# Kernel tuning notes

Hardware: AMD Instinct MI355X
Metric: run time of the kernel (lower is better)

The kernel has to match this reference:

```python
import jax, jax.numpy as jnp
import numpy as np

B, S, D = 4, 2048, 1024
H, HD = 16, 64
SCALE = 1.0 / np.sqrt(HD)


def setup_inputs() -> dict:
    key = jax.random.key(0)
    k1, k2, k3 = jax.random.split(key, 3)
    std = 0.02
    return {
        "hidden_states": jax.random.normal(k1, (B, S, D), jnp.float32),
        "attention_mask": jnp.ones((B, S), dtype=bool),
        "w_attn": jax.random.normal(k2, (D, 3 * D), jnp.float32) * std,
        "b_attn": jnp.zeros((3 * D,), jnp.float32),
        "w_proj": jax.random.normal(k3, (D, D), jnp.float32) * std,
        "b_proj": jnp.zeros((D,), jnp.float32),
    }


def reference(hidden_states, attention_mask, w_attn, b_attn, w_proj, b_proj):
    b, s, _ = hidden_states.shape
    qkv = hidden_states @ w_attn + b_attn                     # [B,S,3D]
    q, k, v = jnp.split(qkv, 3, axis=-1)
    # [B,H,S,HD]
    q = q.reshape(b, s, H, HD).transpose(0, 2, 1, 3)
    k = k.reshape(b, s, H, HD).transpose(0, 2, 1, 3)
    v = v.reshape(b, s, H, HD).transpose(0, 2, 1, 3)
    scores = jnp.einsum('bhqd,bhkd->bhqk', q, k) * SCALE      # [B,H,S,S]
    causal = jnp.tril(jnp.ones((s, s), dtype=bool))
    scores = jnp.where(causal, scores, -jnp.inf)
    scores = jnp.where(attention_mask[:, None, None, :], scores, -jnp.inf)
    probs = jax.nn.softmax(scores, axis=-1)
    out = jnp.einsum('bhqk,bhkd->bhqd', probs, v)             # [B,H,S,HD]
    out = out.transpose(0, 2, 1, 3).reshape(b, s, H * HD)
    return out @ w_proj + b_proj
```

## Files before the change

### kernel.cpp

```cpp
#include <hip/hip_runtime.h>
#include <hip/hip_bf16.h>
#include <stdint.h>

#define B_ 4
#define S_ 2048
#define D_ 1024
#define H_ 16
#define HD_ 64
#define TD_ 3072
#define SCALE_ 0.125f
#define SC2_ 0.18033688011112042f
#define KVB 64
#define QB 128

typedef __attribute__((ext_vector_type(4))) float f32x4;
typedef __attribute__((ext_vector_type(16))) float f32x16;
typedef __attribute__((ext_vector_type(8))) short s16x8;
typedef __attribute__((ext_vector_type(8))) unsigned short u16x8;
typedef __attribute__((ext_vector_type(4))) unsigned int u32x4;

typedef const __attribute__((address_space(1))) unsigned int* gas1p;
typedef __attribute__((address_space(3))) unsigned int* as3p;

__device__ inline void gload_lds16(const void* g, void* l) {
    __builtin_amdgcn_global_load_lds((gas1p)g, (as3p)l, 16, 0, 0);
}

__device__ inline unsigned short f2bf(float f) {
    unsigned u = __builtin_bit_cast(unsigned, f);
    u += 0x7FFFu + ((u >> 16) & 1u);
    return (unsigned short)(u >> 16);
}
__device__ inline float bf2f(unsigned short b) {
    unsigned u = ((unsigned)b) << 16;
    return __builtin_bit_cast(float, u);
}
__device__ inline unsigned cvtpk_bf16(float lo, float hi) {
    unsigned r;
    asm("v_cvt_pk_bf16_f32 %0, %1, %2" : "=v"(r) : "v"(lo), "v"(hi));
    return r;
}
__device__ inline float ex2(float x) { return __builtin_amdgcn_exp2f(x); }

__global__ void sniff_kernel(const unsigned* __restrict__ x, int* __restrict__ flag) {
    int lane = threadIdx.x;
    int cnt = 0;
#pragma unroll
    for (int i = 0; i < 8; i++) {
        unsigned e = (x[lane * 8 + i] >> 7) & 0xFFu;
        cnt += (e > 100u && e < 140u) ? 1 : 0;
    }
    cnt += __shfl_xor(cnt, 1);
    cnt += __shfl_xor(cnt, 2);
    cnt += __shfl_xor(cnt, 4);
    cnt += __shfl_xor(cnt, 8);
    cnt += __shfl_xor(cnt, 16);
    cnt += __shfl_xor(cnt, 32);
    if (lane == 0) *flag = (cnt > 300) ? 1 : 0;
}

__global__ void cvt_bf16_kernel(const void* __restrict__ in, unsigned short* __restrict__ out,
                                long n8, const int* __restrict__ flag) {
    bool isbf = (*flag) != 0;
    long i = (long)blockIdx.x * blockDim.x + threadIdx.x;
    long stride = (long)gridDim.x * blockDim.x;
    for (; i < n8; i += stride) {
        if (isbf) {
            ((u32x4*)out)[i] = ((const u32x4*)in)[i];
        } else {
            const float* f = (const float*)in + i * 8;
            u16x8 r;
#pragma unroll
            for (int j = 0; j < 8; j++) r[j] = f2bf(f[j]);
            ((u16x8*)out)[i] = r;
        }
    }
}

__global__ void tcvt2_kernel(const void* __restrict__ in0, unsigned short* __restrict__ out0,
                             const void* __restrict__ in1, unsigned short* __restrict__ out1,
                             const int* __restrict__ flag) {
    int z = blockIdx.z;
    int bx = blockIdx.x, by = blockIdx.y;
    if (z == 1 && bx >= 32) return;
    const void* in = z ? in1 : in0;
    unsigned short* out = z ? out1 : out0;
    int R = 1024;
    int C = z ? 1024 : 3072;
    bool isbf = (*flag) != 0;
    __shared__ unsigned short tile[32][33];
    int x = threadIdx.x, y0 = threadIdx.y;
    int c = bx * 32 + x;
    for (int yy = y0; yy < 32; yy += 8) {
        long r = by * 32 + yy;
        unsigned short v;
        if (isbf) v = ((const unsigned short*)in)[r * C + c];
        else      v = f2bf(((const float*)in)[r * C + c]);
        tile[yy][x] = v;
    }
    __syncthreads();
    for (int yy = y0; yy < 32; yy += 8) {
        out[(long)(bx * 32 + yy) * R + by * 32 + x] = tile[x][yy];
    }
}

__global__ void cvt_bias_kernel(const void* __restrict__ in0, float* __restrict__ out0,
                                const void* __restrict__ in1, float* __restrict__ out1,
                                const int* __restrict__ flag) {
    bool isbf = (*flag) != 0;
    int i = blockIdx.x * blockDim.x + threadIdx.x;
    if (i < 3072) {
        out0[i] = isbf ? bf2f(((const unsigned short*)in0)[i]) : ((const float*)in0)[i];
    } else if (i < 4096) {
        int j = i - 3072;
        out1[j] = isbf ? bf2f(((const unsigned short*)in1)[j]) : ((const float*)in1)[j];
    }
}

__global__ __launch_bounds__(512)
void vtrans_kernel(const unsigned short* __restrict__ QKV, unsigned short* __restrict__ Vt) {
    __shared__ unsigned short tile[64][72];
    int t = threadIdx.x;
    int st = blockIdx.x;
    int bh = blockIdx.y;
    int b = bh >> 4, h = bh & 15;
    const unsigned short* src = QKV + (long)b * S_ * TD_ + 2 * D_ + h * HD_;
    int sr = t >> 3, d0 = (t & 7) * 8;
    u16x8 v = *(const u16x8*)(src + (long)(st * 64 + sr) * TD_ + d0);
    *(u16x8*)&tile[sr][d0] = v;
    __syncthreads();
    int dr = t >> 3, s0 = (t & 7) * 8;
    u16x8 o;
#pragma unroll
    for (int j = 0; j < 8; j++) o[j] = tile[s0 + j][dr];
    *(u16x8*)(Vt + ((long)bh * 64 + dr) * S_ + st * 64 + s0) = o;
}

__global__ __launch_bounds__(256)
void gemm_bt_kernel(const unsigned short* __restrict__ A,
                    const unsigned short* __restrict__ Bt,
                    const float* __restrict__ bias,
                    void* __restrict__ Cout,
                    int M, int N, int K, const int* __restrict__ flag) {
    __shared__ unsigned short As[128 * 32];
    __shared__ unsigned short Bs[128 * 32];
    int t = threadIdx.x;
    int lane = t & 63;
    int w = t >> 6, wr = w >> 1, wc = w & 1;
    int g = lane >> 4, x = lane & 15;

    int nbx = gridDim.x, nby = gridDim.y;
    int nwg = nbx * nby;
    int orig = blockIdx.x + nbx * blockIdx.y;
    int per = nwg >> 3;
    int idx = (orig & 7) * per + (orig >> 3);
    int bx = idx / nby;
    int by = idx - bx * nby;

    long rm = (long)bx * 128;
    long rn = (long)by * 128;
    const char* Ab = (const char*)(A + rm * K);
    const char* Bb = (const char*)(Bt + rn * K);
    int r0 = t >> 2;
    int c0 = (t & 3) * 16;
    long Kb = (long)K * 2;

    f32x4 acc[4][4] = {};

    for (int k0 = 0; k0 < K; k0 += 32) {
        __syncthreads();
        long kb = (long)k0 * 2;
        gload_lds16(Ab + (long)r0 * Kb + kb + c0,        (char*)As + t * 16);
        gload_lds16(Ab + (long)(r0 + 64) * Kb + kb + c0, (char*)As + t * 16 + 4096);
        gload_lds16(Bb + (long)r0 * Kb + kb + c0,        (char*)Bs + t * 16);
        gload_lds16(Bb + (long)(r0 + 64) * Kb + kb + c0, (char*)Bs + t * 16 + 4096);
        __syncthreads();

        s16x8 af[4], bfr[4];
#pragma unroll
        for (int m = 0; m < 4; m++) af[m]  = *(const s16x8*)&As[(wr * 64 + m * 16 + x) * 32 + g * 8];
#pragma unroll
        for (int n = 0; n < 4; n++) bfr[n] = *(const s16x8*)&Bs[(wc * 64 + n * 16 + x) * 32 + g * 8];
#pragma unroll
        for (int m = 0; m < 4; m++)
#pragma unroll
            for (int n = 0; n < 4; n++)
                acc[m][n] = __builtin_amdgcn_mfma_f32_16x16x32_bf16(af[m], bfr[n], acc[m][n], 0, 0, 0);
    }

    bool f32out = flag ? ((*flag) == 0) : false;
    float bv[4];
#pragma unroll
    for (int n = 0; n < 4; n++) bv[n] = bias[rn + wc * 64 + n * 16 + x];

#pragma unroll
    for (int m = 0; m < 4; m++) {
#pragma unroll
        for (int r = 0; r < 4; r++) {
            long row = rm + wr * 64 + m * 16 + g * 4 + r;
            if (f32out) {
                float* cp = (float*)Cout + row * N;
#pragma unroll
                for (int n = 0; n < 4; n++) cp[rn + wc * 64 + n * 16 + x] = acc[m][n][r] + bv[n];
            } else {
                unsigned short* cp = (unsigned short*)Cout + row * N;
#pragma unroll
                for (int n = 0; n < 4; n++) cp[rn + wc * 64 + n * 16 + x] = f2bf(acc[m][n][r] + bv[n]);
            }
        }
    }
}

__global__ __launch_bounds__(256)
void attn_kernel(const unsigned short* __restrict__ QKV,
                 const unsigned short* __restrict__ Vt_g,
                 unsigned short* __restrict__ O) {
    __shared__ unsigned short Ks[2][64 * 64];
    __shared__ unsigned short Vs[2][64 * 64];

    int t = threadIdx.x, lane = t & 63, w = t >> 6;
    int hi = lane >> 5, q32 = lane & 31;
    int b = blockIdx.z, h = blockIdx.y;
    int pair = blockIdx.x;

    const unsigned short* base = QKV + (long)b * S_ * TD_;
    const unsigned short* Kb = base + D_ + h * HD_;
    const unsigned short* Vb = Vt_g + (long)(b * H_ + h) * HD_ * S_;

    int srow = t >> 3;
    int scol = (((t & 7) ^ (srow & 7)) << 3);

#define STAGE(bi, kt_)                                                            \
    {                                                                             \
        int ks_ = (kt_) * KVB;                                                    \
        gload_lds16(Kb + (long)(ks_ + srow) * TD_ + scol,      (char*)Ks[bi] + t * 16);          \
        gload_lds16(Kb + (long)(ks_ + 32 + srow) * TD_ + scol, (char*)Ks[bi] + 4096 + t * 16);   \
        gload_lds16(Vb + (long)srow * S_ + ks_ + scol,         (char*)Vs[bi] + t * 16);          \
        gload_lds16(Vb + (long)(32 + srow) * S_ + ks_ + scol,  (char*)Vs[bi] + 4096 + t * 16);   \
    }

    for (int ph = 0; ph < 2; ph++) {
        int qt = ph ? (15 - pair) : pair;
        int q0 = qt * QB;
        int q0w = q0 + w * 32;
        int nt = 2 * qt + 2;
        int wlimit = q0w + 31;
        int qg = q0w + q32;

        s16x8 qf[4];
        {
            const unsigned short* qr = base + (long)(q0w + q32) * TD_ + h * HD_;
#pragma unroll
            for (int ds = 0; ds < 4; ds++) {
                u16x8 qraw = *(const u16x8*)(qr + ds * 16 + hi * 8);
                u16x8 qs;
#pragma unroll
                for (int j = 0; j < 8; j++) qs[j] = f2bf(bf2f(qraw[j]) * SC2_);
                qf[ds] = __builtin_bit_cast(s16x8, qs);
            }
        }

        f32x16 acc0 = {}, acc1 = {};
        float sv[8] = {};

        STAGE(0, 0);
        __syncthreads();

        for (int kt = 0; kt < nt; kt++) {
            int bi = kt & 1;
            int ks = kt * KVB;
            if (kt + 1 < nt) STAGE(bi ^ 1, kt + 1);

            if (ks <= wlimit) {
                const char* KsB = (const char*)Ks[bi];
                const char* VsB = (const char*)Vs[bi];

                f32x16 sf0 = {}, sf1 = {};
                __builtin_amdgcn_s_setprio(1);
#pragma unroll
                for (int ds = 0; ds < 4; ds++) {
                    int krow0 = q32;
                    int krow1 = 32 + q32;
                    s16x8 kf0 = *(const s16x8*)(KsB + krow0 * 128 + (((ds * 2 + hi) ^ (krow0 & 7)) << 4));
                    s16x8 kf1 = *(const s16x8*)(KsB + krow1 * 128 + (((ds * 2 + hi) ^ (krow1 & 7)) << 4));
                    sf0 = __builtin_amdgcn_mfma_f32_32x32x16_bf16(kf0, qf[ds], sf0, 0, 0, 0);
                    sf1 = __builtin_amdgcn_mfma_f32_32x32x16_bf16(kf1, qf[ds], sf1, 0, 0, 0);
                }
                __builtin_amdgcn_s_setprio(0);

                if (ks + 63 > q0w) {
#pragma unroll
                    for (int r = 0; r < 16; r++) {
                        int koff = (r & 3) + 8 * (r >> 2) + 4 * hi;
                        if (ks + koff > qg)      sf0[r] = -__builtin_inff();
                        if (ks + 32 + koff > qg) sf1[r] = -__builtin_inff();
                    }
                }

#pragma unroll
                for (int r = 0; r < 16; r++) {
                    sf0[r] = ex2(sf0[r]);
                    sf1[r] = ex2(sf1[r]);
                }
#pragma unroll
                for (int r = 0; r < 8; r++)
                    sv[r] += (sf0[r] + sf0[r + 8]) + (sf1[r] + sf1[r + 8]);

                __builtin_amdgcn_s_setprio(1);
#pragma unroll
                for (int kst = 0; kst < 4; kst++) {
                    unsigned w00, w01, w10, w11;
                    if (kst == 0) { w00=cvtpk_bf16(sf0[0],sf0[1]);  w01=cvtpk_bf16(sf0[2],sf0[3]);
                                    w10=cvtpk_bf16(sf0[4],sf0[5]);  w11=cvtpk_bf16(sf0[6],sf0[7]); }
                    else if (kst == 1) { w00=cvtpk_bf16(sf0[8],sf0[9]);   w01=cvtpk_bf16(sf0[10],sf0[11]);
                                         w10=cvtpk_bf16(sf0[12],sf0[13]); w11=cvtpk_bf16(sf0[14],sf0[15]); }
                    else if (kst == 2) { w00=cvtpk_bf16(sf1[0],sf1[1]);  w01=cvtpk_bf16(sf1[2],sf1[3]);
                                         w10=cvtpk_bf16(sf1[4],sf1[5]);  w11=cvtpk_bf16(sf1[6],sf1[7]); }
                    else { w00=cvtpk_bf16(sf1[8],sf1[9]);   w01=cvtpk_bf16(sf1[10],sf1[11]);
                           w10=cvtpk_bf16(sf1[12],sf1[13]); w11=cvtpk_bf16(sf1[14],sf1[15]); }
                    auto sA = __builtin_amdgcn_permlane32_swap(w00, w10, false, false);
                    auto sB = __builtin_amdgcn_permlane32_swap(w01, w11, false, false);
                    union { unsigned u[4]; s16x8 v; } pa;
                    pa.u[0] = sA[0]; pa.u[1] = sB[0]; pa.u[2] = sA[1]; pa.u[3] = sB[1];

                    int d0 = q32;
                    int d1 = 32 + q32;
                    s16x8 vf0 = *(const s16x8*)(VsB + d0 * 128 + (((kst * 2 + hi) ^ (d0 & 7)) << 4));
                    s16x8 vf1 = *(const s16x8*)(VsB + d1 * 128 + (((kst * 2 + hi) ^ (d1 & 7)) << 4));
                    acc0 = __builtin_amdgcn_mfma_f32_32x32x16_bf16(pa.v, vf0, acc0, 0, 0, 0);
                    acc1 = __builtin_amdgcn_mfma_f32_32x32x16_bf16(pa.v, vf1, acc1, 0, 0, 0);
                }
                __builtin_amdgcn_s_setprio(0);
            }
            __syncthreads();
        }

        float dl = ((sv[0] + sv[1]) + (sv[2] + sv[3])) + ((sv[4] + sv[5]) + (sv[6] + sv[7]));
        float denom = dl + __shfl_xor(dl, 32);
        float inv = 1.0f / denom;

#pragma unroll
        for (int r = 0; r < 16; r++) {
            int crow = (r & 3) + 8 * (r >> 2) + 4 * hi;
            float ir = __shfl(inv, crow);
            long row = (long)b * S_ + q0w + crow;
            O[row * D_ + h * HD_ + q32]      = f2bf(acc0[r] * ir);
            O[row * D_ + h * HD_ + 32 + q32] = f2bf(acc1[r] * ir);
        }
    }
#undef STAGE
}

extern "C" void kernel_launch(void* const* d_in, const int* in_sizes, int n_in,
                              void* d_out, int out_size, void* d_ws, size_t ws_size,
                              hipStream_t stream) {
    char* ws = (char*)d_ws;
    int* flag            = (int*)ws;
    unsigned short* Xb   = (unsigned short*)(ws + 256);
    unsigned short* W1t  = Xb + 8192L * 1024;
    unsigned short* QKV  = W1t + 3072L * 1024;
    unsigned short* W2t  = QKV + 8192L * 3072;
    unsigned short* Ob   = W2t + 1024L * 1024;
    unsigned short* Vt_g = Ob + 8192L * 1024;
    float* b1            = (float*)(Vt_g + 64L * 64 * 2048);
    float* b2            = b1 + 3072;

    sniff_kernel<<<1, 64, 0, stream>>>((const unsigned*)d_in[0], flag);

    cvt_bf16_kernel<<<2048, 256, 0, stream>>>(d_in[0], Xb, 8192L * 1024 / 8, flag);
    tcvt2_kernel<<<dim3(96, 32, 2), dim3(32, 8), 0, stream>>>(d_in[2], W1t, d_in[4], W2t, flag);
    cvt_bias_kernel<<<16, 256, 0, stream>>>(d_in[3], b1, d_in[5], b2, flag);

    gemm_bt_kernel<<<dim3(64, 24), 256, 0, stream>>>(Xb, W1t, b1, QKV, 8192, 3072, 1024, nullptr);

    vtrans_kernel<<<dim3(32, 64), 512, 0, stream>>>(QKV, Vt_g);

    attn_kernel<<<dim3(8, 16, 4), 256, 0, stream>>>(QKV, Vt_g, Ob);

    gemm_bt_kernel<<<dim3(64, 8), 256, 0, stream>>>(Ob, W2t, b2, d_out, 8192, 1024, 1024, flag);
}
```

Measured before the change: 282.3 us.

## Fuse V transpose into QKV GEMM epilogue, swizzle LDS, skip bf16 copy

Removes the separate V-transpose kernel by having the QKV GEMM write V tiles straight into the transposed Vt buffer from its epilogue. It also adds an XOR swizzle to the GEMM's LDS layout to reduce bank conflicts on fragment reads. When the input is already bf16, the conversion kernel now returns early and the GEMM reads the original input directly instead of a copy. The V-tile blocks now do narrow 8-byte strided stores into Vt, which may coalesce less well than the old transpose kernel's writes.

Result: faster. 272.3 us (-3.5%).

```diff
diff --git a/kernel.cpp b/kernel.cpp
--- a/kernel.cpp
+++ b/kernel.cpp
@@ -17,6 +17,7 @@
 typedef __attribute__((ext_vector_type(16))) float f32x16;
 typedef __attribute__((ext_vector_type(8))) short s16x8;
 typedef __attribute__((ext_vector_type(8))) unsigned short u16x8;
+typedef __attribute__((ext_vector_type(4))) unsigned short u16x4;
 typedef __attribute__((ext_vector_type(4))) unsigned int u32x4;
 
 typedef const __attribute__((address_space(1))) unsigned int* gas1p;
@@ -61,19 +62,15 @@
 
 __global__ void cvt_bf16_kernel(const void* __restrict__ in, unsigned short* __restrict__ out,
                                 long n8, const int* __restrict__ flag) {
-    bool isbf = (*flag) != 0;
+    if ((*flag) != 0) return;
     long i = (long)blockIdx.x * blockDim.x + threadIdx.x;
     long stride = (long)gridDim.x * blockDim.x;
     for (; i < n8; i += stride) {
-        if (isbf) {
-            ((u32x4*)out)[i] = ((const u32x4*)in)[i];
-        } else {
-            const float* f = (const float*)in + i * 8;
-            u16x8 r;
-#pragma unroll
-            for (int j = 0; j < 8; j++) r[j] = f2bf(f[j]);
-            ((u16x8*)out)[i] = r;
-        }
+        const float* f = (const float*)in + i * 8;
+        u16x8 r;
+#pragma unroll
+        for (int j = 0; j < 8; j++) r[j] = f2bf(f[j]);
+        ((u16x8*)out)[i] = r;
     }
 }
 
@@ -117,37 +114,24 @@
     }
 }
 
-__global__ __launch_bounds__(512)
-void vtrans_kernel(const unsigned short* __restrict__ QKV, unsigned short* __restrict__ Vt) {
-    __shared__ unsigned short tile[64][72];
-    int t = threadIdx.x;
-    int st = blockIdx.x;
-    int bh = blockIdx.y;
-    int b = bh >> 4, h = bh & 15;
-    const unsigned short* src = QKV + (long)b * S_ * TD_ + 2 * D_ + h * HD_;
-    int sr = t >> 3, d0 = (t & 7) * 8;
-    u16x8 v = *(const u16x8*)(src + (long)(st * 64 + sr) * TD_ + d0);
-    *(u16x8*)&tile[sr][d0] = v;
-    __syncthreads();
-    int dr = t >> 3, s0 = (t & 7) * 8;
-    u16x8 o;
-#pragma unroll
-    for (int j = 0; j < 8; j++) o[j] = tile[s0 + j][dr];
-    *(u16x8*)(Vt + ((long)bh * 64 + dr) * S_ + st * 64 + s0) = o;
-}
-
 __global__ __launch_bounds__(256)
 void gemm_bt_kernel(const unsigned short* __restrict__ A,
+                    const unsigned short* __restrict__ Aalt,
                     const unsigned short* __restrict__ Bt,
                     const float* __restrict__ bias,
                     void* __restrict__ Cout,
-                    int M, int N, int K, const int* __restrict__ flag) {
+                    int M, int N, int K,
+                    const int* __restrict__ flag, int f32sel,
+                    unsigned short* __restrict__ Vt) {
     __shared__ unsigned short As[128 * 32];
     __shared__ unsigned short Bs[128 * 32];
     int t = threadIdx.x;
     int lane = t & 63;
     int w = t >> 6, wr = w >> 1, wc = w & 1;
     int g = lane >> 4, x = lane & 15;
+
+    int fl = flag ? *flag : 1;
+    const unsigned short* Ause = fl ? Aalt : A;
 
     int nbx = gridDim.x, nby = gridDim.y;
     int nwg = nbx * nby;
@@ -159,11 +143,12 @@
 
     long rm = (long)bx * 128;
     long rn = (long)by * 128;
-    const char* Ab = (const char*)(A + rm * K);
+    const char* Ab = (const char*)(Ause + rm * K);
     const char* Bb = (const char*)(Bt + rn * K);
     int r0 = t >> 2;
-    int c0 = (t & 3) * 16;
+    int c0 = (((t & 3) ^ ((r0 >> 1) & 3)) * 16);
     long Kb = (long)K * 2;
+    int swz = (x >> 1) & 3;
 
     f32x4 acc[4][4] = {};
 
@@ -178,9 +163,11 @@
 
         s16x8 af[4], bfr[4];
 #pragma unroll
-        for (int m = 0; m < 4; m++) af[m]  = *(const s16x8*)&As[(wr * 64 + m * 16 + x) * 32 + g * 8];
-#pragma unroll
-        for (int n = 0; n < 4; n++) bfr[n] = *(const s16x8*)&Bs[(wc * 64 + n * 16 + x) * 32 + g * 8];
+        for (int m = 0; m < 4; m++)
+            af[m]  = *(const s16x8*)((const char*)As + (wr * 64 + m * 16 + x) * 64 + ((g ^ swz) << 4));
+#pragma unroll
+        for (int n = 0; n < 4; n++)
+            bfr[n] = *(const s16x8*)((const char*)Bs + (wc * 64 + n * 16 + x) * 64 + ((g ^ swz) << 4));
 #pragma unroll
         for (int m = 0; m < 4; m++)
 #pragma unroll
@@ -188,11 +175,27 @@
                 acc[m][n] = __builtin_amdgcn_mfma_f32_16x16x32_bf16(af[m], bfr[n], acc[m][n], 0, 0, 0);
     }
 
-    bool f32out = flag ? ((*flag) == 0) : false;
     float bv[4];
 #pragma unroll
     for (int n = 0; n < 4; n++) bv[n] = bias[rn + wc * 64 + n * 16 + x];
 
+    if (Vt != nullptr && rn >= 2048) {
+        long vrow = ((rm >> 11) << 4) + ((rn - 2048) >> 6) + wc;
+        int sbase = (int)(rm & 2047) + wr * 64 + g * 4;
+#pragma unroll
+        for (int m = 0; m < 4; m++) {
+#pragma unroll
+            for (int n = 0; n < 4; n++) {
+                u16x4 pk;
+#pragma unroll
+                for (int r = 0; r < 4; r++) pk[r] = f2bf(acc[m][n][r] + bv[n]);
+                *(u16x4*)&Vt[(vrow * 64 + n * 16 + x) * 2048 + sbase + m * 16] = pk;
+            }
+        }
+        return;
+    }
+
+    bool f32out = (f32sel != 0) && (fl == 0);
 #pragma unroll
     for (int m = 0; m < 4; m++) {
 #pragma unroll
@@ -371,11 +374,11 @@
     tcvt2_kernel<<<dim3(96, 32, 2), dim3(32, 8), 0, stream>>>(d_in[2], W1t, d_in[4], W2t, flag);
     cvt_bias_kernel<<<16, 256, 0, stream>>>(d_in[3], b1, d_in[5], b2, flag);
 
-    gemm_bt_kernel<<<dim3(64, 24), 256, 0, stream>>>(Xb, W1t, b1, QKV, 8192, 3072, 1024, nullptr);
-
-    vtrans_kernel<<<dim3(32, 64), 512, 0, stream>>>(QKV, Vt_g);
+    gemm_bt_kernel<<<dim3(64, 24), 256, 0, stream>>>(
+        Xb, (const unsigned short*)d_in[0], W1t, b1, QKV, 8192, 3072, 1024, flag, 0, Vt_g);
 
     attn_kernel<<<dim3(8, 16, 4), 256, 0, stream>>>(QKV, Vt_g, Ob);
 
-    gemm_bt_kernel<<<dim3(64, 8), 256, 0, stream>>>(Ob, W2t, b2, d_out, 8192, 1024, 1024, flag);
-}
+    gemm_bt_kernel<<<dim3(64, 8), 256, 0, stream>>>(
+        Ob, Ob, W2t, b2, d_out, 8192, 1024, 1024, flag, 1, nullptr);
+}
```
